# Kernel optimization log

Measured on AMD Instinct MI355X. Metric: run time of the kernel, lower is better.

The kernel has to match this reference:

```python
import jax, jax.numpy as jnp
import numpy as np

B, L, D, H = 2, 2048, 1024, 16
HD = D // H  # head dim = 64


def setup_inputs() -> dict:
    key = jax.random.key(0)
    ks = jax.random.split(key, 5)
    s = 1.0 / np.sqrt(D)
    return {
        "x": jax.random.normal(ks[0], (B, L, D), dtype=jnp.float32),
        "mask": jnp.ones((B, 1, 1, L), dtype=jnp.int32),
        "Wq": jax.random.normal(ks[1], (D, D), dtype=jnp.float32) * s,
        "bq": jnp.zeros((D,), dtype=jnp.float32),
        "Wk": jax.random.normal(ks[2], (D, D), dtype=jnp.float32) * s,
        "bk": jnp.zeros((D,), dtype=jnp.float32),
        "Wv": jax.random.normal(ks[3], (D, D), dtype=jnp.float32) * s,
        "bv": jnp.zeros((D,), dtype=jnp.float32),
        "Wo": jax.random.normal(ks[4], (D, D), dtype=jnp.float32) * s,
        "bo": jnp.zeros((D,), dtype=jnp.float32),
    }


def reference(x, mask, Wq, bq, Wk, bk, Wv, bv, Wo, bo):
    Bx, Lx = x.shape[0], x.shape[1]
    # torch nn.Linear: y = x @ W.T + b
    q = (jnp.einsum("bld,ed->ble", x, Wq) + bq).reshape(Bx, Lx, H, HD).transpose(0, 2, 1, 3)
    k = (jnp.einsum("bld,ed->ble", x, Wk) + bk).reshape(Bx, Lx, H, HD).transpose(0, 2, 1, 3)
    v = (jnp.einsum("bld,ed->ble", x, Wv) + bv).reshape(Bx, Lx, H, HD).transpose(0, 2, 1, 3)
    # [B, H, L, L] scores
    scores = jnp.einsum("bhqd,bhkd->bhqk", q, k) / np.sqrt(HD).astype(np.float32)
    # faithful to original: masked positions are set to the tiny value 1e-9 (not -inf)
    scores = jnp.where(mask == 0, jnp.float32(1e-9), scores)
    attn = jax.nn.softmax(scores, axis=-1)
    # dropout_prob=0.0 -> identity (eval mode)
    out = jnp.einsum("bhqk,bhkd->bhqd", attn, v)  # [B, H, L, HD]
    out = out.transpose(0, 2, 1, 3).reshape(Bx, Lx, D)
    return jnp.einsum("bld,ed->ble", out, Wo) + bo
```

## Files before the change

### kernel.cpp

```cpp
#include <hip/hip_runtime.h>
#include <hip/hip_bf16.h>

typedef _Float16 f16;
typedef _Float16 f16x8 __attribute__((ext_vector_type(8)));
typedef _Float16 f16x4 __attribute__((ext_vector_type(4)));
typedef float f32x4 __attribute__((ext_vector_type(4)));

#define LDS_LOAD16(gptr, lptr)                                                             \
  __builtin_amdgcn_global_load_lds(                                                        \
      (const __attribute__((address_space(1))) unsigned int*)(gptr),                       \
      (__attribute__((address_space(3))) unsigned int*)(lptr), 16, 0, 0)

#define ALPHA 0.18033688f

__global__ __launch_bounds__(256) void conv_all(const float* __restrict__ x,
                                                const float* __restrict__ Wq,
                                                const float* __restrict__ Wk,
                                                const float* __restrict__ Wv,
                                                const float* __restrict__ Wo,
                                                f16* __restrict__ xh, f16* __restrict__ wqh,
                                                f16* __restrict__ wkh, f16* __restrict__ wvh,
                                                f16* __restrict__ woh) {
  int i = blockIdx.x * 256 + threadIdx.x;
  const float* src;
  f16* dst;
  int off;
  if (i < 524288) {
    src = x; dst = xh; off = i;
  } else {
    int j = i - 524288;
    int w = j >> 17;
    off = j & 131071;
    src = (w == 0) ? Wq : (w == 1) ? Wk : (w == 2) ? Wv : Wo;
    dst = (w == 0) ? wqh : (w == 1) ? wkh : (w == 2) ? wvh : woh;
  }
  const float4* s4 = (const float4*)src;
  float4 a = s4[2 * off];
  float4 b = s4[2 * off + 1];
  f16x8 o = {(f16)a.x, (f16)a.y, (f16)a.z, (f16)a.w,
             (f16)b.x, (f16)b.y, (f16)b.z, (f16)b.w};
  *(f16x8*)(dst + (size_t)off * 8) = o;
}

__global__ __launch_bounds__(256) void gemm_qkv(const f16* __restrict__ A,
                                                const f16* __restrict__ W0,
                                                const f16* __restrict__ W1,
                                                const f16* __restrict__ W2,
                                                const float* __restrict__ b0,
                                                const float* __restrict__ b1,
                                                const float* __restrict__ b2,
                                                f16* __restrict__ qo, f16* __restrict__ ko,
                                                f16* __restrict__ vo) {
  constexpr int K = 1024, BM = 128, BK = 32;
  __shared__ f16 aT[BM * BK];
  __shared__ f16 bT[BM * BK];
  const int z = blockIdx.z;
  const f16* Bw = (z == 0) ? W0 : (z == 1) ? W1 : W2;
  const float* bias = (z == 0) ? b0 : (z == 1) ? b1 : b2;
  const int tid = threadIdx.x, wid = tid >> 6, lane = tid & 63;
  const int mb = blockIdx.y * BM, nb = blockIdx.x * BM;
  const int wr = wid >> 1, wc = wid & 1;
  const int lr = lane & 15, hi = lane >> 4;

  f32x4 acc[4][4] = {};

  const int r0 = tid >> 2, s0 = tid & 3;
  const int ci1 = 256 + tid, r1 = ci1 >> 2, s1 = ci1 & 3;

  for (int kt = 0; kt < K / BK; ++kt) {
    __syncthreads();
    const int kb = kt * BK;
    LDS_LOAD16(A + (size_t)(mb + r0) * K + kb + s0 * 8, (char*)aT + wid * 1024);
    LDS_LOAD16(Bw + (size_t)(nb + r0) * K + kb + s0 * 8, (char*)bT + wid * 1024);
    LDS_LOAD16(A + (size_t)(mb + r1) * K + kb + s1 * 8, (char*)aT + 4096 + wid * 1024);
    LDS_LOAD16(Bw + (size_t)(nb + r1) * K + kb + s1 * 8, (char*)bT + 4096 + wid * 1024);
    __syncthreads();

    f16x8 af[4], bf[4];
#pragma unroll
    for (int i = 0; i < 4; ++i) af[i] = *(const f16x8*)&aT[(wr * 64 + i * 16 + lr) * BK + hi * 8];
#pragma unroll
    for (int j = 0; j < 4; ++j) bf[j] = *(const f16x8*)&bT[(wc * 64 + j * 16 + lr) * BK + hi * 8];
    __builtin_amdgcn_s_setprio(1);
#pragma unroll
    for (int i = 0; i < 4; ++i)
#pragma unroll
      for (int j = 0; j < 4; ++j)
        acc[i][j] = __builtin_amdgcn_mfma_f32_16x16x32_f16(af[i], bf[j], acc[i][j], 0, 0, 0);
    __builtin_amdgcn_s_setprio(0);
  }

  const float scale = (z == 0) ? ALPHA : 1.0f;
#pragma unroll
  for (int i = 0; i < 4; ++i) {
#pragma unroll
    for (int j = 0; j < 4; ++j) {
      const int row = mb + wr * 64 + i * 16 + hi * 4;
      const int col = nb + wc * 64 + j * 16 + lr;
      const float bv = bias[col];
      const int hh = col >> 6, dd = col & 63;
      if (z == 2) {
        const int bb = row >> 11, l = row & 2047;
        f16x4 v4;
#pragma unroll
        for (int r = 0; r < 4; ++r) v4[r] = (f16)(acc[i][j][r] + bv);
        *(f16x4*)(vo + ((((size_t)bb * 16 + hh) * 64 + dd) * 2048 + l)) = v4;
      } else {
        f16* o = z ? ko : qo;
#pragma unroll
        for (int r = 0; r < 4; ++r) {
          const int m2 = row + r;
          const int bb = m2 >> 11, l = m2 & 2047;
          o[((((size_t)bb * 16 + hh) * 2048 + l) * 64) + dd] = (f16)((acc[i][j][r] + bv) * scale);
        }
      }
    }
  }
}

__global__ __launch_bounds__(256) void gemm_out(const f16* __restrict__ A,
                                                const f16* __restrict__ W,
                                                const float* __restrict__ bias,
                                                float* __restrict__ out) {
  constexpr int K = 1024, N = 1024, BK = 32;
  __shared__ f16 aT[64 * BK];
  __shared__ f16 bT[64 * BK];
  const int tid = threadIdx.x, wid = tid >> 6, lane = tid & 63;
  const int lr = lane & 15, hi = lane >> 4;
  const int mb = blockIdx.y * 64, nb = blockIdx.x * 64;
  f32x4 acc[4] = {};
  const int r0 = tid >> 2, s0 = tid & 3;

  for (int kt = 0; kt < K / BK; ++kt) {
    __syncthreads();
    const int kb = kt * BK;
    LDS_LOAD16(A + (size_t)(mb + r0) * K + kb + s0 * 8, (char*)aT + wid * 1024);
    LDS_LOAD16(W + (size_t)(nb + r0) * K + kb + s0 * 8, (char*)bT + wid * 1024);
    __syncthreads();
    f16x8 af = *(const f16x8*)&aT[(wid * 16 + lr) * BK + hi * 8];
    __builtin_amdgcn_s_setprio(1);
#pragma unroll
    for (int j = 0; j < 4; ++j) {
      f16x8 bf = *(const f16x8*)&bT[(j * 16 + lr) * BK + hi * 8];
      acc[j] = __builtin_amdgcn_mfma_f32_16x16x32_f16(af, bf, acc[j], 0, 0, 0);
    }
    __builtin_amdgcn_s_setprio(0);
  }
#pragma unroll
  for (int j = 0; j < 4; ++j) {
    const int col = nb + j * 16 + lr;
    const float bv = bias[col];
#pragma unroll
    for (int r = 0; r < 4; ++r)
      out[(size_t)(mb + wid * 16 + hi * 4 + r) * N + col] = acc[j][r] + bv;
  }
}

__global__ __launch_bounds__(256) void attn64(const f16* __restrict__ Qh,
                                              const f16* __restrict__ Kh,
                                              const f16* __restrict__ Vt,
                                              const int* __restrict__ mask,
                                              f16* __restrict__ Oa) {
  constexpr int L = 2048, HD = 64, H = 16;
  __shared__ f16 kT[64 * 64];
  __shared__ f16 vT[64 * 64];
  __shared__ f16 pT[4 * 16 * 64];

  const int tid = threadIdx.x, wid = tid >> 6, lane = tid & 63;
  const int bh = blockIdx.y, b = bh >> 4, h = bh & 15;
  const int lr = lane & 15, hi = lane >> 4;
  const int xr = (lr & 7) << 4;

  const f16* Qb = Qh + (size_t)bh * L * HD;
  const f16* Kb = Kh + (size_t)bh * L * HD;
  const f16* Vb = Vt + (size_t)bh * HD * L;
  const int* mrow = mask + b * L;

  const int qr = blockIdx.x * 64 + wid * 16;
  const f16x8 qf0 = *(const f16x8*)&Qb[(size_t)(qr + lr) * HD + hi * 8];
  const f16x8 qf1 = *(const f16x8*)&Qb[(size_t)(qr + lr) * HD + 32 + hi * 8];

  f32x4 oacc[4] = {};
  float lsum[4] = {0.f, 0.f, 0.f, 0.f};

  const int kr0 = tid >> 3, ks0 = (tid & 7) ^ (kr0 & 7);
  const int ci1 = 256 + tid;
  const int kr1 = ci1 >> 3, ks1 = (ci1 & 7) ^ (kr1 & 7);

  char* kTb = (char*)kT;
  char* vTb = (char*)vT;
  char* pTb = (char*)pT + wid * 2048;

  for (int kt = 0; kt < L / 64; ++kt) {
    __syncthreads();
    LDS_LOAD16(Kb + (size_t)(kt * 64 + kr0) * HD + ks0 * 8, kTb + wid * 1024);
    LDS_LOAD16(Vb + (size_t)kr0 * L + kt * 64 + ks0 * 8, vTb + wid * 1024);
    LDS_LOAD16(Kb + (size_t)(kt * 64 + kr1) * HD + ks1 * 8, kTb + 4096 + wid * 1024);
    LDS_LOAD16(Vb + (size_t)kr1 * L + kt * 64 + ks1 * 8, vTb + 4096 + wid * 1024);
    __syncthreads();

    f32x4 s[4];
    __builtin_amdgcn_s_setprio(1);
#pragma unroll
    for (int nf = 0; nf < 4; ++nf) {
      const char* krow = kTb + (nf * 16 + lr) * 128;
      f16x8 kf0 = *(const f16x8*)(krow + ((hi * 16) ^ xr));
      f16x8 kf1 = *(const f16x8*)(krow + ((hi * 16) ^ xr ^ 64));
      f32x4 z = {-8.f, -8.f, -8.f, -8.f};
      z = __builtin_amdgcn_mfma_f32_16x16x32_f16(qf0, kf0, z, 0, 0, 0);
      z = __builtin_amdgcn_mfma_f32_16x16x32_f16(qf1, kf1, z, 0, 0, 0);
      s[nf] = z;
    }
    __builtin_amdgcn_s_setprio(0);

#pragma unroll
    for (int nf = 0; nf < 4; ++nf) {
      const int mv = mrow[kt * 64 + nf * 16 + lr];
#pragma unroll
      for (int r = 0; r < 4; ++r) {
        float t = mv ? s[nf][r] : (1.44269504e-9f - 8.0f);
        float p = __builtin_amdgcn_exp2f(t);
        lsum[r] += p;
        const int qrow = hi * 4 + r;
        *(f16*)(pTb + qrow * 128 + ((nf * 32 + lr * 2) ^ ((qrow & 7) << 4))) = (f16)p;
      }
    }

    __builtin_amdgcn_s_setprio(1);
#pragma unroll
    for (int kh = 0; kh < 2; ++kh) {
      f16x8 pf = *(const f16x8*)(pTb + lr * 128 + (((4 * kh + hi) * 16) ^ xr));
#pragma unroll
      for (int df = 0; df < 4; ++df) {
        f16x8 vf = *(const f16x8*)(vTb + (df * 16 + lr) * 128 + (((4 * kh + hi) * 16) ^ xr));
        oacc[df] = __builtin_amdgcn_mfma_f32_16x16x32_f16(pf, vf, oacc[df], 0, 0, 0);
      }
    }
    __builtin_amdgcn_s_setprio(0);
  }

#pragma unroll
  for (int r = 0; r < 4; ++r) {
    float t = lsum[r];
    t += __shfl_xor(t, 1);
    t += __shfl_xor(t, 2);
    t += __shfl_xor(t, 4);
    t += __shfl_xor(t, 8);
    lsum[r] = 1.0f / t;
  }
#pragma unroll
  for (int df = 0; df < 4; ++df)
#pragma unroll
    for (int r = 0; r < 4; ++r) {
      const int l = qr + hi * 4 + r;
      Oa[(((size_t)b * L + l) * H + h) * HD + df * 16 + lr] = (f16)(oacc[df][r] * lsum[r]);
    }
}

extern "C" void kernel_launch(void* const* d_in, const int* in_sizes, int n_in,
                              void* d_out, int out_size, void* d_ws, size_t ws_size,
                              hipStream_t stream) {
  const float* x  = (const float*)d_in[0];
  const int* mask = (const int*)d_in[1];
  const float* Wq = (const float*)d_in[2];
  const float* bq = (const float*)d_in[3];
  const float* Wk = (const float*)d_in[4];
  const float* bk = (const float*)d_in[5];
  const float* Wv = (const float*)d_in[6];
  const float* bv = (const float*)d_in[7];
  const float* Wo = (const float*)d_in[8];
  const float* bo = (const float*)d_in[9];
  float* out = (float*)d_out;

  char* ws = (char*)d_ws;
  const size_t MB = 1u << 20;
  f16* xh  = (f16*)(ws);
  f16* wqh = (f16*)(ws + 8 * MB);
  f16* wkh = (f16*)(ws + 10 * MB);
  f16* wvh = (f16*)(ws + 12 * MB);
  f16* woh = (f16*)(ws + 14 * MB);
  f16* qh  = (f16*)(ws + 16 * MB);
  f16* kh  = (f16*)(ws + 24 * MB);
  f16* vth = (f16*)(ws + 32 * MB);
  f16* oah = (f16*)(ws + 40 * MB);

  conv_all<<<4096, 256, 0, stream>>>(x, Wq, Wk, Wv, Wo, xh, wqh, wkh, wvh, woh);

  gemm_qkv<<<dim3(8, 32, 3), 256, 0, stream>>>(xh, wqh, wkh, wvh, bq, bk, bv, qh, kh, vth);

  attn64<<<dim3(2048 / 64, 32), 256, 0, stream>>>(qh, kh, vth, mask, oah);

  gemm_out<<<dim3(16, 64), 256, 0, stream>>>(oah, woh, bo, out);
}
```

Measured before the change: 130.1 us.

## Enlarge attention query tile, double-buffer K/V loads, widen output GEMM tile

The attention kernel now handles 128 query rows per block (32 per wave), so each K/V tile loaded into LDS is reused across twice as many queries. K/V loads are double-buffered so the next tile's global-to-LDS copy overlaps the current tile's compute, leaving one barrier per iteration. The output projection GEMM moves to 64x128 block tiles with a 2x4 MFMA fragment grid per wave, giving more reuse per LDS load. The trade-off is fewer blocks (512 for attention), which means less occupancy slack, plus higher register and LDS use.

```diff
diff --git a/kernel.cpp b/kernel.cpp
--- a/kernel.cpp
+++ b/kernel.cpp
@@ -118,143 +118,186 @@
   }
 }
 
-__global__ __launch_bounds__(256) void gemm_out(const f16* __restrict__ A,
-                                                const f16* __restrict__ W,
-                                                const float* __restrict__ bias,
-                                                float* __restrict__ out) {
+__global__ __launch_bounds__(256) void gemm_o(const f16* __restrict__ A,
+                                              const f16* __restrict__ W,
+                                              const float* __restrict__ bias,
+                                              float* __restrict__ out) {
   constexpr int K = 1024, N = 1024, BK = 32;
   __shared__ f16 aT[64 * BK];
-  __shared__ f16 bT[64 * BK];
+  __shared__ f16 bT[128 * BK];
   const int tid = threadIdx.x, wid = tid >> 6, lane = tid & 63;
   const int lr = lane & 15, hi = lane >> 4;
-  const int mb = blockIdx.y * 64, nb = blockIdx.x * 64;
-  f32x4 acc[4] = {};
-  const int r0 = tid >> 2, s0 = tid & 3;
+  const int mb = blockIdx.y * 64, nb = blockIdx.x * 128;
+  const int wr = wid >> 1, wc = wid & 1;
+  f32x4 acc[2][4] = {};
+  const int ra = tid >> 2, sa = tid & 3;
+  const int rb1 = (256 + tid) >> 2, sb1 = (256 + tid) & 3;
 
   for (int kt = 0; kt < K / BK; ++kt) {
     __syncthreads();
     const int kb = kt * BK;
-    LDS_LOAD16(A + (size_t)(mb + r0) * K + kb + s0 * 8, (char*)aT + wid * 1024);
-    LDS_LOAD16(W + (size_t)(nb + r0) * K + kb + s0 * 8, (char*)bT + wid * 1024);
-    __syncthreads();
-    f16x8 af = *(const f16x8*)&aT[(wid * 16 + lr) * BK + hi * 8];
+    LDS_LOAD16(A + (size_t)(mb + ra) * K + kb + sa * 8, (char*)aT + wid * 1024);
+    LDS_LOAD16(W + (size_t)(nb + ra) * K + kb + sa * 8, (char*)bT + wid * 1024);
+    LDS_LOAD16(W + (size_t)(nb + rb1) * K + kb + sb1 * 8, (char*)bT + 4096 + wid * 1024);
+    __syncthreads();
+    f16x8 af[2], bf[4];
+#pragma unroll
+    for (int i = 0; i < 2; ++i) af[i] = *(const f16x8*)&aT[(wr * 32 + i * 16 + lr) * BK + hi * 8];
+#pragma unroll
+    for (int j = 0; j < 4; ++j) bf[j] = *(const f16x8*)&bT[(wc * 64 + j * 16 + lr) * BK + hi * 8];
     __builtin_amdgcn_s_setprio(1);
 #pragma unroll
+    for (int i = 0; i < 2; ++i)
+#pragma unroll
+      for (int j = 0; j < 4; ++j)
+        acc[i][j] = __builtin_amdgcn_mfma_f32_16x16x32_f16(af[i], bf[j], acc[i][j], 0, 0, 0);
+    __builtin_amdgcn_s_setprio(0);
+  }
+#pragma unroll
+  for (int i = 0; i < 2; ++i)
+#pragma unroll
     for (int j = 0; j < 4; ++j) {
-      f16x8 bf = *(const f16x8*)&bT[(j * 16 + lr) * BK + hi * 8];
-      acc[j] = __builtin_amdgcn_mfma_f32_16x16x32_f16(af, bf, acc[j], 0, 0, 0);
+      const int col = nb + wc * 64 + j * 16 + lr;
+      const float bv = bias[col];
+#pragma unroll
+      for (int r = 0; r < 4; ++r)
+        out[(size_t)(mb + wr * 32 + i * 16 + hi * 4 + r) * N + col] = acc[i][j][r] + bv;
     }
-    __builtin_amdgcn_s_setprio(0);
-  }
-#pragma unroll
-  for (int j = 0; j < 4; ++j) {
-    const int col = nb + j * 16 + lr;
-    const float bv = bias[col];
-#pragma unroll
-    for (int r = 0; r < 4; ++r)
-      out[(size_t)(mb + wid * 16 + hi * 4 + r) * N + col] = acc[j][r] + bv;
-  }
-}
-
-__global__ __launch_bounds__(256) void attn64(const f16* __restrict__ Qh,
-                                              const f16* __restrict__ Kh,
-                                              const f16* __restrict__ Vt,
-                                              const int* __restrict__ mask,
-                                              f16* __restrict__ Oa) {
+}
+
+__global__ __launch_bounds__(256) void attn128(const f16* __restrict__ Qh,
+                                               const f16* __restrict__ Kh,
+                                               const f16* __restrict__ Vt,
+                                               const int* __restrict__ mask,
+                                               f16* __restrict__ Oa) {
   constexpr int L = 2048, HD = 64, H = 16;
-  __shared__ f16 kT[64 * 64];
-  __shared__ f16 vT[64 * 64];
-  __shared__ f16 pT[4 * 16 * 64];
+  __shared__ f16 kT[2][64 * 64];
+  __shared__ f16 vT[2][64 * 64];
+  __shared__ f16 pT[4][32 * 64];
 
   const int tid = threadIdx.x, wid = tid >> 6, lane = tid & 63;
   const int bh = blockIdx.y, b = bh >> 4, h = bh & 15;
   const int lr = lane & 15, hi = lane >> 4;
-  const int xr = (lr & 7) << 4;
+  const int sw = lr & 7;
 
   const f16* Qb = Qh + (size_t)bh * L * HD;
   const f16* Kb = Kh + (size_t)bh * L * HD;
   const f16* Vb = Vt + (size_t)bh * HD * L;
   const int* mrow = mask + b * L;
 
-  const int qr = blockIdx.x * 64 + wid * 16;
-  const f16x8 qf0 = *(const f16x8*)&Qb[(size_t)(qr + lr) * HD + hi * 8];
-  const f16x8 qf1 = *(const f16x8*)&Qb[(size_t)(qr + lr) * HD + 32 + hi * 8];
-
-  f32x4 oacc[4] = {};
-  float lsum[4] = {0.f, 0.f, 0.f, 0.f};
+  const int qr0 = blockIdx.x * 128 + wid * 32;
+  f16x8 qf[2][2];
+#pragma unroll
+  for (int qg = 0; qg < 2; ++qg)
+#pragma unroll
+    for (int kh = 0; kh < 2; ++kh)
+      qf[qg][kh] = *(const f16x8*)&Qb[(size_t)(qr0 + qg * 16 + lr) * HD + kh * 32 + hi * 8];
+
+  f32x4 oacc[2][4] = {};
+  float lsum[2][4] = {};
 
   const int kr0 = tid >> 3, ks0 = (tid & 7) ^ (kr0 & 7);
-  const int ci1 = 256 + tid;
-  const int kr1 = ci1 >> 3, ks1 = (ci1 & 7) ^ (kr1 & 7);
-
-  char* kTb = (char*)kT;
-  char* vTb = (char*)vT;
-  char* pTb = (char*)pT + wid * 2048;
+  const int ci1 = 256 + tid, kr1 = ci1 >> 3, ks1 = (ci1 & 7) ^ (kr1 & 7);
+  char* pTb = (char*)pT + wid * 4096;
+
+#define STAGE(bb, kt)                                                                        \
+  do {                                                                                       \
+    LDS_LOAD16(Kb + (size_t)((kt) * 64 + kr0) * HD + ks0 * 8,                                \
+               (char*)kT + (bb) * 8192 + wid * 1024);                                        \
+    LDS_LOAD16(Vb + (size_t)kr0 * L + (kt) * 64 + ks0 * 8,                                   \
+               (char*)vT + (bb) * 8192 + wid * 1024);                                        \
+    LDS_LOAD16(Kb + (size_t)((kt) * 64 + kr1) * HD + ks1 * 8,                                \
+               (char*)kT + (bb) * 8192 + 4096 + wid * 1024);                                 \
+    LDS_LOAD16(Vb + (size_t)kr1 * L + (kt) * 64 + ks1 * 8,                                   \
+               (char*)vT + (bb) * 8192 + 4096 + wid * 1024);                                 \
+  } while (0)
+
+  STAGE(0, 0);
+  __syncthreads();
+  int buf = 0;
 
   for (int kt = 0; kt < L / 64; ++kt) {
-    __syncthreads();
-    LDS_LOAD16(Kb + (size_t)(kt * 64 + kr0) * HD + ks0 * 8, kTb + wid * 1024);
-    LDS_LOAD16(Vb + (size_t)kr0 * L + kt * 64 + ks0 * 8, vTb + wid * 1024);
-    LDS_LOAD16(Kb + (size_t)(kt * 64 + kr1) * HD + ks1 * 8, kTb + 4096 + wid * 1024);
-    LDS_LOAD16(Vb + (size_t)kr1 * L + kt * 64 + ks1 * 8, vTb + 4096 + wid * 1024);
-    __syncthreads();
-
-    f32x4 s[4];
+    if (kt + 1 < L / 64) STAGE(buf ^ 1, kt + 1);
+    const char* kB = (char*)kT + buf * 8192;
+    const char* vB = (char*)vT + buf * 8192;
+
+    f16x8 kf[4][2];
+#pragma unroll
+    for (int nf = 0; nf < 4; ++nf)
+#pragma unroll
+      for (int k2 = 0; k2 < 2; ++k2)
+        kf[nf][k2] = *(const f16x8*)(kB + (nf * 16 + lr) * 128 + ((k2 * 4 + hi) ^ sw) * 16);
+
+    f32x4 s[2][4];
     __builtin_amdgcn_s_setprio(1);
 #pragma unroll
-    for (int nf = 0; nf < 4; ++nf) {
-      const char* krow = kTb + (nf * 16 + lr) * 128;
-      f16x8 kf0 = *(const f16x8*)(krow + ((hi * 16) ^ xr));
-      f16x8 kf1 = *(const f16x8*)(krow + ((hi * 16) ^ xr ^ 64));
-      f32x4 z = {-8.f, -8.f, -8.f, -8.f};
-      z = __builtin_amdgcn_mfma_f32_16x16x32_f16(qf0, kf0, z, 0, 0, 0);
-      z = __builtin_amdgcn_mfma_f32_16x16x32_f16(qf1, kf1, z, 0, 0, 0);
-      s[nf] = z;
-    }
+    for (int qg = 0; qg < 2; ++qg)
+#pragma unroll
+      for (int nf = 0; nf < 4; ++nf) {
+        f32x4 z = {-8.f, -8.f, -8.f, -8.f};
+        z = __builtin_amdgcn_mfma_f32_16x16x32_f16(qf[qg][0], kf[nf][0], z, 0, 0, 0);
+        z = __builtin_amdgcn_mfma_f32_16x16x32_f16(qf[qg][1], kf[nf][1], z, 0, 0, 0);
+        s[qg][nf] = z;
+      }
     __builtin_amdgcn_s_setprio(0);
 
 #pragma unroll
     for (int nf = 0; nf < 4; ++nf) {
       const int mv = mrow[kt * 64 + nf * 16 + lr];
 #pragma unroll
+      for (int qg = 0; qg < 2; ++qg)
+#pragma unroll
+        for (int r = 0; r < 4; ++r) {
+          float t = mv ? s[qg][nf][r] : (1.44269504e-9f - 8.0f);
+          float p = __builtin_amdgcn_exp2f(t);
+          lsum[qg][r] += p;
+          const int row = qg * 16 + hi * 4 + r;
+          *(f16*)(pTb + row * 128 + ((nf * 32 + lr * 2) ^ ((row & 7) << 4))) = (f16)p;
+        }
+    }
+
+    f16x8 pf[2][2];
+#pragma unroll
+    for (int qg = 0; qg < 2; ++qg)
+#pragma unroll
+      for (int k2 = 0; k2 < 2; ++k2)
+        pf[qg][k2] = *(const f16x8*)(pTb + (qg * 16 + lr) * 128 + ((k2 * 4 + hi) ^ sw) * 16);
+    __builtin_amdgcn_s_setprio(1);
+#pragma unroll
+    for (int k2 = 0; k2 < 2; ++k2)
+#pragma unroll
+      for (int df = 0; df < 4; ++df) {
+        f16x8 vf = *(const f16x8*)(vB + (df * 16 + lr) * 128 + ((k2 * 4 + hi) ^ sw) * 16);
+        oacc[0][df] = __builtin_amdgcn_mfma_f32_16x16x32_f16(pf[0][k2], vf, oacc[0][df], 0, 0, 0);
+        oacc[1][df] = __builtin_amdgcn_mfma_f32_16x16x32_f16(pf[1][k2], vf, oacc[1][df], 0, 0, 0);
+      }
+    __builtin_amdgcn_s_setprio(0);
+
+    __syncthreads();
+    buf ^= 1;
+  }
+
+#pragma unroll
+  for (int qg = 0; qg < 2; ++qg)
+#pragma unroll
+    for (int r = 0; r < 4; ++r) {
+      float t = lsum[qg][r];
+      t += __shfl_xor(t, 1);
+      t += __shfl_xor(t, 2);
+      t += __shfl_xor(t, 4);
+      t += __shfl_xor(t, 8);
+      lsum[qg][r] = 1.0f / t;
+    }
+#pragma unroll
+  for (int qg = 0; qg < 2; ++qg)
+#pragma unroll
+    for (int df = 0; df < 4; ++df)
+#pragma unroll
       for (int r = 0; r < 4; ++r) {
-        float t = mv ? s[nf][r] : (1.44269504e-9f - 8.0f);
-        float p = __builtin_amdgcn_exp2f(t);
-        lsum[r] += p;
-        const int qrow = hi * 4 + r;
-        *(f16*)(pTb + qrow * 128 + ((nf * 32 + lr * 2) ^ ((qrow & 7) << 4))) = (f16)p;
+        const int l = qr0 + qg * 16 + hi * 4 + r;
+        Oa[(((size_t)b * L + l) * H + h) * HD + df * 16 + lr] =
+            (f16)(oacc[qg][df][r] * lsum[qg][r]);
       }
-    }
-
-    __builtin_amdgcn_s_setprio(1);
-#pragma unroll
-    for (int kh = 0; kh < 2; ++kh) {
-      f16x8 pf = *(const f16x8*)(pTb + lr * 128 + (((4 * kh + hi) * 16) ^ xr));
-#pragma unroll
-      for (int df = 0; df < 4; ++df) {
-        f16x8 vf = *(const f16x8*)(vTb + (df * 16 + lr) * 128 + (((4 * kh + hi) * 16) ^ xr));
-        oacc[df] = __builtin_amdgcn_mfma_f32_16x16x32_f16(pf, vf, oacc[df], 0, 0, 0);
-      }
-    }
-    __builtin_amdgcn_s_setprio(0);
-  }
-
-#pragma unroll
-  for (int r = 0; r < 4; ++r) {
-    float t = lsum[r];
-    t += __shfl_xor(t, 1);
-    t += __shfl_xor(t, 2);
-    t += __shfl_xor(t, 4);
-    t += __shfl_xor(t, 8);
-    lsum[r] = 1.0f / t;
-  }
-#pragma unroll
-  for (int df = 0; df < 4; ++df)
-#pragma unroll
-    for (int r = 0; r < 4; ++r) {
-      const int l = qr + hi * 4 + r;
-      Oa[(((size_t)b * L + l) * H + h) * HD + df * 16 + lr] = (f16)(oacc[df][r] * lsum[r]);
-    }
 }
 
 extern "C" void kernel_launch(void* const* d_in, const int* in_sizes, int n_in,
@@ -288,7 +331,7 @@
 
   gemm_qkv<<<dim3(8, 32, 3), 256, 0, stream>>>(xh, wqh, wkh, wvh, bq, bk, bv, qh, kh, vth);
 
-  attn64<<<dim3(2048 / 64, 32), 256, 0, stream>>>(qh, kh, vth, mask, oah);
-
-  gemm_out<<<dim3(16, 64), 256, 0, stream>>>(oah, woh, bo, out);
-}
+  attn128<<<dim3(16, 32), 256, 0, stream>>>(qh, kh, vth, mask, oah);
+
+  gemm_o<<<dim3(8, 64), 256, 0, stream>>>(oah, woh, bo, out);
+}
```

Measured after the change: 136.7 us. 5.1% more time.
